# Kernel tuning notes

Measured on AMD Instinct MI355X. Metric: run time of the kernel, lower is better.

## Reference

```python
import jax, jax.numpy as jnp
import numpy as np

B, T = 2, 2048
N_EMBED = 2048
N_HEAD = 16
N_KV_HEAD = 4
HEAD_DIM = N_EMBED // N_HEAD  # 128
KV_DIM = HEAD_DIM * N_KV_HEAD  # 512
REPEAT = N_HEAD // N_KV_HEAD  # 4
THETA = 10000.0


def _apply_rope(x):
    # x: (B, T, H, D), interleaved-pair rotation as in RotaryEmbedding
    D = x.shape[-1]
    inv_freq = 1.0 / (THETA ** (jnp.arange(0, D, 2, dtype=jnp.float32) / D))  # (D/2,)
    t = jnp.arange(x.shape[1], dtype=jnp.float32)
    freqs = t[:, None] * inv_freq[None, :]            # (T, D/2)
    cos = jnp.cos(freqs)[None, :, None, :]            # (1, T, 1, D/2)
    sin = jnp.sin(freqs)[None, :, None, :]
    x1 = x[..., ::2]
    x2 = x[..., 1::2]
    even = x1 * cos - x2 * sin
    odd = x1 * sin + x2 * cos
    out = jnp.stack([even, odd], axis=-1)             # (B, T, H, D/2, 2)
    return out.reshape(x.shape)


def setup_inputs() -> dict:
    key = jax.random.key(0)
    ks = jax.random.split(key, 9)
    s_in = 1.0 / np.sqrt(N_EMBED)
    return {
        "x": jax.random.normal(ks[0], (B, T, N_EMBED), dtype=jnp.float32),
        "Wq": jax.random.normal(ks[1], (N_EMBED, N_EMBED), dtype=jnp.float32) * s_in,
        "bq": jax.random.normal(ks[2], (N_EMBED,), dtype=jnp.float32) * 0.01,
        "Wk": jax.random.normal(ks[3], (KV_DIM, N_EMBED), dtype=jnp.float32) * s_in,
        "bk": jax.random.normal(ks[4], (KV_DIM,), dtype=jnp.float32) * 0.01,
        "Wv": jax.random.normal(ks[5], (KV_DIM, N_EMBED), dtype=jnp.float32) * s_in,
        "bv": jax.random.normal(ks[6], (KV_DIM,), dtype=jnp.float32) * 0.01,
        "Wo": jax.random.normal(ks[7], (N_EMBED, N_EMBED), dtype=jnp.float32) * s_in,
        "bo": jax.random.normal(ks[8], (N_EMBED,), dtype=jnp.float32) * 0.01,
    }


def reference(x, Wq, bq, Wk, bk, Wv, bv, Wo, bo):
    Bb, Tt, _ = x.shape
    q = (x @ Wq.T + bq).reshape(Bb, Tt, N_HEAD, HEAD_DIM)
    k = (x @ Wk.T + bk).reshape(Bb, Tt, N_KV_HEAD, HEAD_DIM)
    v = (x @ Wv.T + bv).reshape(Bb, Tt, N_KV_HEAD, HEAD_DIM)
    xq = _apply_rope(q).transpose(0, 2, 1, 3)          # (B, H, T, D)
    xk = _apply_rope(k).transpose(0, 2, 1, 3)          # (B, Hkv, T, D)
    xv = v.transpose(0, 2, 1, 3)
    if REPEAT > 1:
        xk = jnp.repeat(xk, REPEAT, axis=1)            # (B, H, T, D)
        xv = jnp.repeat(xv, REPEAT, axis=1)
    qk = jnp.einsum('bhqd,bhkd->bhqk', xq, xk)         # NOTE: no pre-softmax scale (faithful)
    causal = jnp.tril(jnp.ones((Tt, Tt), dtype=bool))
    qk = jnp.where(causal[None, None, :, :], qk, -jnp.inf)
    attn = jax.nn.softmax(qk, axis=-1) * (N_EMBED ** -0.5)  # post-softmax scale, faithful to source
    o = jnp.einsum('bhqk,bhkd->bhqd', attn, xv)
    o = o.transpose(0, 2, 1, 3).reshape(Bb, Tt, N_EMBED)
    return o @ Wo.T + bo
```

## Files before the change

### kernel.cpp

```cpp
#include <hip/hip_runtime.h>
#include <math.h>


typedef __bf16 bf16;
typedef __bf16 bf16x8 __attribute__((ext_vector_type(8)));
typedef __bf16 bf16x4 __attribute__((ext_vector_type(4)));
typedef __bf16 bf16x2 __attribute__((ext_vector_type(2)));
typedef float  f32x4  __attribute__((ext_vector_type(4)));

#define T_SEQ 2048
#define NE    2048
#define NH    16
#define NKVH  4
#define HD    128
#define KVD   512
#define OSCALE 0.022097086912079608f

__device__ __forceinline__ void gload16(const void* g, void* l) {
  __builtin_amdgcn_global_load_lds(
      (const __attribute__((address_space(1))) void*)g,
      (__attribute__((address_space(3))) void*)l, 16, 0, 0);
}

__global__ __launch_bounds__(256) void prep_convert(
    const float* __restrict__ x,  const float* __restrict__ wq,
    const float* __restrict__ wk, const float* __restrict__ wv,
    const float* __restrict__ wo,
    bf16* __restrict__ xb,  bf16* __restrict__ wqb, bf16* __restrict__ wkb,
    bf16* __restrict__ wvb, bf16* __restrict__ wob)
{
  const size_t total4 = (size_t)(8388608 + 4194304 + 1048576 + 1048576 + 4194304) / 4;
  for (size_t i = (size_t)blockIdx.x * blockDim.x + threadIdx.x; i < total4;
       i += (size_t)gridDim.x * blockDim.x) {
    size_t e = i * 4;
    const float* s; bf16* d; size_t off;
    if      (e <  8388608u) { s = x;  d = xb;  off = e; }
    else if (e < 12582912u) { s = wq; d = wqb; off = e -  8388608u; }
    else if (e < 13631488u) { s = wk; d = wkb; off = e - 12582912u; }
    else if (e < 14680064u) { s = wv; d = wvb; off = e - 13631488u; }
    else                    { s = wo; d = wob; off = e - 14680064u; }
    float4 v = *(const float4*)(s + off);
    bf16x4 o = {(bf16)v.x, (bf16)v.y, (bf16)v.z, (bf16)v.w};
    *(bf16x4*)(d + off) = o;
  }
}

__global__ __launch_bounds__(256) void rope_init(float2* __restrict__ rope)
{
  int i = blockIdx.x * 256 + threadIdx.x;
  int t = i >> 6, p = i & 63;
  float invf = powf(10000.f, -(float)p * (1.f / 64.f));
  double frd = (double)((float)t * invf);
  rope[i] = make_float2((float)cos(frd), (float)sin(frd));
}

__device__ __forceinline__ void mfma_gemm_128(
    const bf16* __restrict__ Ag,
    const bf16* __restrict__ Bg,
    f32x4 acc[4][4])
{
  __shared__ bf16 As[128][32];
  __shared__ bf16 Bs[128][32];
  const int tid  = threadIdx.x;
  const int wave = tid >> 6, lane = tid & 63;
  const int g = lane >> 4, c = lane & 15;
  const int wm = wave >> 1, wn = wave & 1;

  const f32x4 zf = {0.f, 0.f, 0.f, 0.f};
  #pragma unroll
  for (int mi = 0; mi < 4; ++mi)
    #pragma unroll
    for (int ni = 0; ni < 4; ++ni) acc[mi][ni] = zf;

  const int lr = lane >> 2;
  const int lc = (lane & 3) * 8;
  const bf16* aG0 = Ag + (size_t)(wave * 16 + lr) * NE + lc;
  const bf16* aG1 = aG0 + (size_t)64 * NE;
  const bf16* bG0 = Bg + (size_t)(wave * 16 + lr) * NE + lc;
  const bf16* bG1 = bG0 + (size_t)64 * NE;
  bf16* aL0 = &As[wave * 16][0];
  bf16* aL1 = &As[64 + wave * 16][0];
  bf16* bL0 = &Bs[wave * 16][0];
  bf16* bL1 = &Bs[64 + wave * 16][0];

  for (int k0 = 0; k0 < NE; k0 += 32) {
    __syncthreads();
    gload16(aG0 + k0, aL0);
    gload16(aG1 + k0, aL1);
    gload16(bG0 + k0, bL0);
    gload16(bG1 + k0, bL1);
    __syncthreads();
    bf16x8 af[4], bfr[4];
    #pragma unroll
    for (int mi = 0; mi < 4; ++mi)
      af[mi] = *(const bf16x8*)&As[wm * 64 + mi * 16 + c][g * 8];
    #pragma unroll
    for (int ni = 0; ni < 4; ++ni)
      bfr[ni] = *(const bf16x8*)&Bs[wn * 64 + ni * 16 + c][g * 8];
    #pragma unroll
    for (int mi = 0; mi < 4; ++mi)
      #pragma unroll
      for (int ni = 0; ni < 4; ++ni)
        acc[mi][ni] = __builtin_amdgcn_mfma_f32_16x16x32_bf16(
            af[mi], bfr[ni], acc[mi][ni], 0, 0, 0);
  }
}

__device__ __forceinline__ int xcd_swz(int bid, int nwg) {
  return (bid & 7) * (nwg >> 3) + (bid >> 3);
}

__global__ __launch_bounds__(256) void qkv_mfma(
    const bf16* __restrict__ xb,  const bf16* __restrict__ wqb,
    const bf16* __restrict__ wkb, const bf16* __restrict__ wvb,
    const float* __restrict__ bq, const float* __restrict__ bk,
    const float* __restrict__ bv, const float2* __restrict__ rope,
    bf16* __restrict__ q_ws, bf16* __restrict__ k_ws, bf16* __restrict__ vT_ws)
{
  const int wid = xcd_swz(blockIdx.x, 768);
  const int n0 = (wid % 24) * 128;
  const int m0 = (wid / 24) * 128;
  int region; const bf16* Wp; const float* bp; int nl0;
  if (n0 < NE)            { region = 0; Wp = wqb; bp = bq; nl0 = n0; }
  else if (n0 < NE + KVD) { region = 1; Wp = wkb; bp = bk; nl0 = n0 - NE; }
  else                    { region = 2; Wp = wvb; bp = bv; nl0 = n0 - NE - KVD; }

  f32x4 acc[4][4];
  mfma_gemm_128(xb + (size_t)m0 * NE, Wp + (size_t)nl0 * NE, acc);

  const int tid = threadIdx.x, wave = tid >> 6, lane = tid & 63;
  const int g = lane >> 4, c = lane & 15;
  const int wm = wave >> 1, wn = wave & 1;
  const int bbase = m0 >> 11;
  const int t0base = (m0 & (T_SEQ - 1)) + wm * 64;

  if (region < 2) {
    bf16* dst = (region == 0) ? q_ws : k_ws;
    const int nheads_stride = (region == 0) ? NH : NKVH;
    #pragma unroll
    for (int ni = 0; ni < 4; ++ni) {
      const int nloc = nl0 + wn * 64 + ni * 16 + c;
      const float bias = bp[nloc];
      const int d  = nloc & (HD - 1);
      const int p  = d >> 1;
      const int hh = nloc >> 7;
      const size_t base = ((size_t)bbase * nheads_stride + hh) * (size_t)T_SEQ * HD;
      #pragma unroll
      for (int mi = 0; mi < 4; ++mi) {
        #pragma unroll
        for (int r = 0; r < 4; ++r) {
          const int t = t0base + mi * 16 + g * 4 + r;
          float val = acc[mi][ni][r] + bias;
          float other = __shfl_xor(val, 1);
          float2 cs = rope[t * 64 + p];
          float res = (c & 1) ? fmaf(other, cs.y, val * cs.x)
                              : fmaf(val, cs.x, -(other * cs.y));
          float rpair = __shfl_xor(res, 1);
          if (!(c & 1)) {
            bf16x2 pk = {(bf16)res, (bf16)rpair};
            *(bf16x2*)&dst[base + (size_t)t * HD + d] = pk;
          }
        }
      }
    }
  } else {
    #pragma unroll
    for (int ni = 0; ni < 4; ++ni) {
      const int nloc = nl0 + wn * 64 + ni * 16 + c;
      const float bias = bp[nloc];
      const int d  = nloc & (HD - 1);
      const int hh = nloc >> 7;
      const size_t vrow = ((size_t)bbase * NKVH + hh) * HD + d;
      #pragma unroll
      for (int mi = 0; mi < 4; ++mi) {
        const int t0 = t0base + mi * 16 + g * 4;
        bf16x4 pk = {(bf16)(acc[mi][ni][0] + bias), (bf16)(acc[mi][ni][1] + bias),
                     (bf16)(acc[mi][ni][2] + bias), (bf16)(acc[mi][ni][3] + bias)};
        *(bf16x4*)&vT_ws[vrow * T_SEQ + t0] = pk;
      }
    }
  }
}

__global__ __launch_bounds__(256, 4) void attn_mfma(
    const bf16* __restrict__ q_ws, const bf16* __restrict__ k_ws,
    const bf16* __restrict__ vT_ws, bf16* __restrict__ o_ws)
{
  __shared__ __align__(16) char smem[40960];
  char* Ks = smem;
  char* Vs = smem + 16384;
  char* Ps = smem + 32768;

  const int tid = threadIdx.x, wave = tid >> 6, lane = tid & 63;
  const int g = lane >> 4, c = lane & 15;
  const int bid = blockIdx.x;
  const int u = bid & 31, v = bid >> 5;
  const int h = u & 15, b = u >> 4;
  const int qt = (v < 16) ? v : (47 - v);
  const int kvh = h >> 2;

  const bf16* Qg = q_ws + (((size_t)b * NH + h) * T_SEQ + qt * 64 + wave * 16) * HD;
  const bf16* Kg = k_ws + ((size_t)b * NKVH + kvh) * (size_t)T_SEQ * HD;
  const bf16* Vg = vT_ws + ((size_t)b * NKVH + kvh) * (size_t)HD * T_SEQ;

  bf16x8 qf[4];
  #pragma unroll
  for (int kc = 0; kc < 4; ++kc)
    qf[kc] = *(const bf16x8*)(Qg + (size_t)c * HD + kc * 32 + g * 8);

  const f32x4 zf = {0.f, 0.f, 0.f, 0.f};
  f32x4 o_acc[8];
  #pragma unroll
  for (int i = 0; i < 8; ++i) o_acc[i] = zf;

  float m_run[4], l_run[4];
  #pragma unroll
  for (int r = 0; r < 4; ++r) { m_run[r] = -1e30f; l_run[r] = 0.f; }

  const int qrow_base = qt * 64 + wave * 16 + g * 4;
  const int ks_row = tid >> 4;
  const int ks_cb  = (tid & 15) * 16;
  const int vs_row = tid >> 3;
  const int vs_cb  = (tid & 7) * 16;
  const int swzc   = (c & 7) << 4;
  const int nkt = qt + 1;

  for (int kt = 0; kt < nkt; ++kt) {
    const int kb0 = kt * 64;
    __syncthreads();
    #pragma unroll
    for (int i = 0; i < 4; ++i) {
      int row = ks_row + i * 16;
      bf16x8 vv = *(const bf16x8*)(Kg + (size_t)(kb0 + row) * HD + (ks_cb >> 1));
      *(bf16x8*)(Ks + row * 256 + (ks_cb ^ ((row & 7) << 4))) = vv;
    }
    #pragma unroll
    for (int i = 0; i < 4; ++i) {
      int d = vs_row + i * 32;
      bf16x8 vv = *(const bf16x8*)(Vg + (size_t)d * T_SEQ + kb0 + (vs_cb >> 1));
      *(bf16x8*)(Vs + d * 128 + (vs_cb ^ ((d & 7) << 4))) = vv;
    }
    __syncthreads();

    f32x4 s[4];
    #pragma unroll
    for (int cf = 0; cf < 4; ++cf) s[cf] = zf;
    __builtin_amdgcn_s_setprio(1);
    #pragma unroll
    for (int cf = 0; cf < 4; ++cf)
      #pragma unroll
      for (int kc = 0; kc < 4; ++kc) {
        bf16x8 kf = *(const bf16x8*)(Ks + (cf * 16 + c) * 256 +
                                     ((kc * 64 + g * 16) ^ swzc));
        s[cf] = __builtin_amdgcn_mfma_f32_16x16x32_bf16(qf[kc], kf, s[cf], 0, 0, 0);
      }
    __builtin_amdgcn_s_setprio(0);

    if (kt == qt) {
      #pragma unroll
      for (int cf = 0; cf < 4; ++cf) {
        int key = kb0 + cf * 16 + c;
        #pragma unroll
        for (int r = 0; r < 4; ++r)
          if (key > qrow_base + r) s[cf][r] = -1e30f;
      }
    }

    float corr[4], mx[4];
    #pragma unroll
    for (int r = 0; r < 4; ++r) {
      float m2 = fmaxf(fmaxf(s[0][r], s[1][r]), fmaxf(s[2][r], s[3][r]));
      m2 = fmaxf(m2, __shfl_xor(m2, 1));
      m2 = fmaxf(m2, __shfl_xor(m2, 2));
      m2 = fmaxf(m2, __shfl_xor(m2, 4));
      m2 = fmaxf(m2, __shfl_xor(m2, 8));
      float mn = fmaxf(m_run[r], m2);
      corr[r] = __expf(m_run[r] - mn);
      m_run[r] = mn;
      mx[r] = mn;
    }
    float rs[4] = {0.f, 0.f, 0.f, 0.f};
    #pragma unroll
    for (int cf = 0; cf < 4; ++cf)
      #pragma unroll
      for (int r = 0; r < 4; ++r) {
        float p = __expf(s[cf][r] - mx[r]);
        s[cf][r] = p;
        rs[r] += p;
      }
    #pragma unroll
    for (int r = 0; r < 4; ++r) {
      float t = rs[r];
      t += __shfl_xor(t, 1); t += __shfl_xor(t, 2);
      t += __shfl_xor(t, 4); t += __shfl_xor(t, 8);
      l_run[r] = l_run[r] * corr[r] + t;
    }

    char* Pw = Ps + wave * 2048;
    #pragma unroll
    for (int cf = 0; cf < 4; ++cf)
      #pragma unroll
      for (int r = 0; r < 4; ++r) {
        int row = g * 4 + r;
        *(bf16*)(Pw + row * 128 + (((cf * 16 + c) * 2) ^ ((row & 7) << 4))) =
            (bf16)s[cf][r];
      }

    #pragma unroll
    for (int d0 = 0; d0 < 8; ++d0)
      #pragma unroll
      for (int r = 0; r < 4; ++r)
        o_acc[d0][r] *= corr[r];

    bf16x8 pa0 = *(const bf16x8*)(Pw + c * 128 + ((g * 16) ^ swzc));
    bf16x8 pa1 = *(const bf16x8*)(Pw + c * 128 + ((64 + g * 16) ^ swzc));
    __builtin_amdgcn_s_setprio(1);
    #pragma unroll
    for (int d0 = 0; d0 < 8; ++d0) {
      bf16x8 v0 = *(const bf16x8*)(Vs + (d0 * 16 + c) * 128 + ((g * 16) ^ swzc));
      bf16x8 v1 = *(const bf16x8*)(Vs + (d0 * 16 + c) * 128 + ((64 + g * 16) ^ swzc));
      o_acc[d0] = __builtin_amdgcn_mfma_f32_16x16x32_bf16(pa0, v0, o_acc[d0], 0, 0, 0);
      o_acc[d0] = __builtin_amdgcn_mfma_f32_16x16x32_bf16(pa1, v1, o_acc[d0], 0, 0, 0);
    }
    __builtin_amdgcn_s_setprio(0);
  }

  float f[4];
  #pragma unroll
  for (int r = 0; r < 4; ++r) f[r] = OSCALE / l_run[r];
  #pragma unroll
  for (int d0 = 0; d0 < 8; ++d0)
    #pragma unroll
    for (int r = 0; r < 4; ++r) {
      float val = o_acc[d0][r] * f[r];
      float pv = __shfl_xor(val, 1);
      if (!(c & 1)) {
        bf16x2 pk = {(bf16)val, (bf16)pv};
        size_t row = (size_t)b * T_SEQ + qt * 64 + wave * 16 + g * 4 + r;
        int col = h * HD + d0 * 16 + c;
        *(bf16x2*)&o_ws[row * NE + col] = pk;
      }
    }
}

__global__ __launch_bounds__(256) void out_proj_mfma(
    const bf16* __restrict__ ob, const bf16* __restrict__ wob,
    const float* __restrict__ bo, float* __restrict__ out)
{
  const int wid = xcd_swz(blockIdx.x, 512);
  const int n0 = (wid % 16) * 128;
  const int m0 = (wid / 16) * 128;
  f32x4 acc[4][4];
  mfma_gemm_128(ob + (size_t)m0 * NE, wob + (size_t)n0 * NE, acc);

  const int tid = threadIdx.x, wave = tid >> 6, lane = tid & 63;
  const int g = lane >> 4, c = lane & 15;
  const int wm = wave >> 1, wn = wave & 1;
  #pragma unroll
  for (int ni = 0; ni < 4; ++ni) {
    const int n = n0 + wn * 64 + ni * 16 + c;
    const float bias = bo[n];
    #pragma unroll
    for (int mi = 0; mi < 4; ++mi)
      #pragma unroll
      for (int r = 0; r < 4; ++r) {
        const int m = m0 + wm * 64 + mi * 16 + g * 4 + r;
        out[(size_t)m * NE + n] = acc[mi][ni][r] + bias;
      }
  }
}

extern "C" void kernel_launch(void* const* d_in, const int* in_sizes, int n_in,
                              void* d_out, int out_size, void* d_ws, size_t ws_size,
                              hipStream_t stream)
{
  const float* x  = (const float*)d_in[0];
  const float* Wq = (const float*)d_in[1];
  const float* bq = (const float*)d_in[2];
  const float* Wk = (const float*)d_in[3];
  const float* bk = (const float*)d_in[4];
  const float* Wv = (const float*)d_in[5];
  const float* bv = (const float*)d_in[6];
  const float* Wo = (const float*)d_in[7];
  const float* bo = (const float*)d_in[8];
  float* out = (float*)d_out;

  bf16* xb    = (bf16*)d_ws;
  bf16* wqb   = xb    + 8388608;
  bf16* wkb   = wqb   + 4194304;
  bf16* wvb   = wkb   + 1048576;
  bf16* wob   = wvb   + 1048576;
  bf16* q_ws  = wob   + 4194304;
  bf16* k_ws  = q_ws  + 8388608;
  bf16* vT_ws = k_ws  + 2097152;
  bf16* o_ws  = vT_ws + 2097152;
  float2* rope = (float2*)(o_ws + 8388608);

  prep_convert<<<2048, 256, 0, stream>>>(x, Wq, Wk, Wv, Wo, xb, wqb, wkb, wvb, wob);
  rope_init<<<512, 256, 0, stream>>>(rope);
  qkv_mfma<<<768, 256, 0, stream>>>(xb, wqb, wkb, wvb, bq, bk, bv, rope,
                                    q_ws, k_ws, vT_ws);
  attn_mfma<<<1024, 256, 0, stream>>>(q_ws, k_ws, vT_ws, o_ws);
  out_proj_mfma<<<512, 256, 0, stream>>>(o_ws, wob, bo, out);
}
```

Before: 449.9 us.

## Prefetch next K/V tile into registers and use lazy softmax rescaling

Next K/V tile is loaded into registers while the current tile is being computed, so global load latency overlaps with MFMA work. The online softmax now rescales the running max and accumulators only when some row's new max exceeds the old one by more than 8, which skips most correction multiplies. The per-tile cross-lane row-sum reduction is deferred to a single reduction at the end. This costs extra registers for the prefetch buffers, which may reduce occupancy, and relies on a bounded exponent range for numerical safety.

Measured after the change: 441.0 us. 2.0% less time.

```diff
diff --git a/kernel.cpp b/kernel.cpp
--- a/kernel.cpp
+++ b/kernel.cpp
@@ -213,9 +213,9 @@
   #pragma unroll
   for (int i = 0; i < 8; ++i) o_acc[i] = zf;
 
-  float m_run[4], l_run[4];
-  #pragma unroll
-  for (int r = 0; r < 4; ++r) { m_run[r] = -1e30f; l_run[r] = 0.f; }
+  float m_run[4], l_part[4];
+  #pragma unroll
+  for (int r = 0; r < 4; ++r) { m_run[r] = -1e30f; l_part[r] = 0.f; }
 
   const int qrow_base = qt * 64 + wave * 16 + g * 4;
   const int ks_row = tid >> 4;
@@ -225,22 +225,46 @@
   const int swzc   = (c & 7) << 4;
   const int nkt = qt + 1;
 
+  bf16x8 kreg[4], vreg[4];
+  #pragma unroll
+  for (int i = 0; i < 4; ++i) {
+    int row = ks_row + i * 16;
+    kreg[i] = *(const bf16x8*)(Kg + (size_t)row * HD + (ks_cb >> 1));
+  }
+  #pragma unroll
+  for (int i = 0; i < 4; ++i) {
+    int d = vs_row + i * 32;
+    vreg[i] = *(const bf16x8*)(Vg + (size_t)d * T_SEQ + (vs_cb >> 1));
+  }
+
   for (int kt = 0; kt < nkt; ++kt) {
     const int kb0 = kt * 64;
     __syncthreads();
     #pragma unroll
     for (int i = 0; i < 4; ++i) {
       int row = ks_row + i * 16;
-      bf16x8 vv = *(const bf16x8*)(Kg + (size_t)(kb0 + row) * HD + (ks_cb >> 1));
-      *(bf16x8*)(Ks + row * 256 + (ks_cb ^ ((row & 7) << 4))) = vv;
+      *(bf16x8*)(Ks + row * 256 + (ks_cb ^ ((row & 7) << 4))) = kreg[i];
     }
     #pragma unroll
     for (int i = 0; i < 4; ++i) {
       int d = vs_row + i * 32;
-      bf16x8 vv = *(const bf16x8*)(Vg + (size_t)d * T_SEQ + kb0 + (vs_cb >> 1));
-      *(bf16x8*)(Vs + d * 128 + (vs_cb ^ ((d & 7) << 4))) = vv;
+      *(bf16x8*)(Vs + d * 128 + (vs_cb ^ ((d & 7) << 4))) = vreg[i];
     }
     __syncthreads();
+
+    if (kt + 1 < nkt) {
+      const int nb0 = kb0 + 64;
+      #pragma unroll
+      for (int i = 0; i < 4; ++i) {
+        int row = ks_row + i * 16;
+        kreg[i] = *(const bf16x8*)(Kg + (size_t)(nb0 + row) * HD + (ks_cb >> 1));
+      }
+      #pragma unroll
+      for (int i = 0; i < 4; ++i) {
+        int d = vs_row + i * 32;
+        vreg[i] = *(const bf16x8*)(Vg + (size_t)d * T_SEQ + nb0 + (vs_cb >> 1));
+      }
+    }
 
     f32x4 s[4];
     #pragma unroll
@@ -266,7 +290,7 @@
       }
     }
 
-    float corr[4], mx[4];
+    float pmax[4];
     #pragma unroll
     for (int r = 0; r < 4; ++r) {
       float m2 = fmaxf(fmaxf(s[0][r], s[1][r]), fmaxf(s[2][r], s[3][r]));
@@ -274,27 +298,29 @@
       m2 = fmaxf(m2, __shfl_xor(m2, 2));
       m2 = fmaxf(m2, __shfl_xor(m2, 4));
       m2 = fmaxf(m2, __shfl_xor(m2, 8));
-      float mn = fmaxf(m_run[r], m2);
-      corr[r] = __expf(m_run[r] - mn);
-      m_run[r] = mn;
-      mx[r] = mn;
-    }
-    float rs[4] = {0.f, 0.f, 0.f, 0.f};
+      pmax[r] = m2;
+    }
+    int ok = (pmax[0] <= m_run[0] + 8.f) & (pmax[1] <= m_run[1] + 8.f) &
+             (pmax[2] <= m_run[2] + 8.f) & (pmax[3] <= m_run[3] + 8.f);
+    if (!__all(ok)) {
+      #pragma unroll
+      for (int r = 0; r < 4; ++r) {
+        float mn = fmaxf(m_run[r], pmax[r]);
+        float corr = __expf(m_run[r] - mn);
+        m_run[r] = mn;
+        l_part[r] *= corr;
+        #pragma unroll
+        for (int d0 = 0; d0 < 8; ++d0) o_acc[d0][r] *= corr;
+      }
+    }
     #pragma unroll
     for (int cf = 0; cf < 4; ++cf)
       #pragma unroll
       for (int r = 0; r < 4; ++r) {
-        float p = __expf(s[cf][r] - mx[r]);
+        float p = __expf(s[cf][r] - m_run[r]);
         s[cf][r] = p;
-        rs[r] += p;
-      }
-    #pragma unroll
-    for (int r = 0; r < 4; ++r) {
-      float t = rs[r];
-      t += __shfl_xor(t, 1); t += __shfl_xor(t, 2);
-      t += __shfl_xor(t, 4); t += __shfl_xor(t, 8);
-      l_run[r] = l_run[r] * corr[r] + t;
-    }
+        l_part[r] += p;
+      }
 
     char* Pw = Ps + wave * 2048;
     #pragma unroll
@@ -305,12 +331,6 @@
         *(bf16*)(Pw + row * 128 + (((cf * 16 + c) * 2) ^ ((row & 7) << 4))) =
             (bf16)s[cf][r];
       }
-
-    #pragma unroll
-    for (int d0 = 0; d0 < 8; ++d0)
-      #pragma unroll
-      for (int r = 0; r < 4; ++r)
-        o_acc[d0][r] *= corr[r];
 
     bf16x8 pa0 = *(const bf16x8*)(Pw + c * 128 + ((g * 16) ^ swzc));
     bf16x8 pa1 = *(const bf16x8*)(Pw + c * 128 + ((64 + g * 16) ^ swzc));
@@ -327,7 +347,12 @@
 
   float f[4];
   #pragma unroll
-  for (int r = 0; r < 4; ++r) f[r] = OSCALE / l_run[r];
+  for (int r = 0; r < 4; ++r) {
+    float lt = l_part[r];
+    lt += __shfl_xor(lt, 1); lt += __shfl_xor(lt, 2);
+    lt += __shfl_xor(lt, 4); lt += __shfl_xor(lt, 8);
+    f[r] = OSCALE / lt;
+  }
   #pragma unroll
   for (int d0 = 0; d0 < 8; ++d0)
     #pragma unroll
```
